# Performance work log

Measured on AMD Instinct MI355X. Metric: run time of the kernel, lower is better.

The kernel has to match this reference:

```python
import jax, jax.numpy as jnp
import numpy as np

N_NODES = 10000
N_EDGES = 640000
IN_FEATS = 128
OUT_FEATS = 128


def setup_inputs() -> dict:
    key = jax.random.key(0)
    k1, k2, k3, k4, k5 = jax.random.split(key, 5)
    x = jax.random.normal(k1, (N_NODES, IN_FEATS), dtype=jnp.float32)
    src = jax.random.randint(k2, (N_EDGES,), 0, N_NODES, dtype=jnp.int64)
    dst = jax.random.randint(k3, (N_EDGES,), 0, N_NODES, dtype=jnp.int64)
    # nn.Linear(in_feats, out_feats): weight [out, in], bias [out]
    bound = 1.0 / np.sqrt(IN_FEATS)
    W = jax.random.uniform(k4, (OUT_FEATS, IN_FEATS), minval=-bound, maxval=bound, dtype=jnp.float32)
    b = jax.random.uniform(k5, (OUT_FEATS,), minval=-bound, maxval=bound, dtype=jnp.float32)
    return {"x": x, "src": src, "dst": dst, "W": W, "b": b}


def reference(x, src, dst, W, b):
    # DGL GINConv (eps=0, sum aggregator): rst = (1+eps)*x + sum_{j->i} x_j, then Linear
    agg = jax.ops.segment_sum(x[src], dst, num_segments=N_NODES)  # [N, in]
    h = x + agg
    return h @ W.T + b  # [N, out]
```

## Files before the change

### kernel.cpp

```cpp
#include <hip/hip_runtime.h>

#define N_NODES 10000
#define N_EDGES 640000
#define FEATS 128
#define NBKT 625
#define CAPB 2048
#define GSTRIDE 16
#define GEMM_WAVES 625
#define GEMM_GRID 157
#define P1_BLOCKS 79
#define WCVT_BLOCKS 16
#define XCVT_BLOCKS 1250
#define CLR_BLOCKS 40

typedef __attribute__((ext_vector_type(8))) short short8;
typedef __attribute__((ext_vector_type(4))) float f32x4;

static __device__ __forceinline__ unsigned short f2bf(float f) {
    unsigned int u = __float_as_uint(f);
    u = (u + 0x7FFFu + ((u >> 16) & 1u)) >> 16;
    return (unsigned short)u;
}
static __device__ __forceinline__ float bf2f(unsigned short h) {
    return __uint_as_float((unsigned int)h << 16);
}

__global__ void prep_kernel(const float* __restrict__ x,
                            const float* __restrict__ W,
                            unsigned short* __restrict__ xhi,
                            unsigned short* __restrict__ xlo,
                            unsigned short* __restrict__ wb,
                            int* __restrict__ gcur) {
    int blk = blockIdx.x;
    int tid = threadIdx.x;
    if (blk < WCVT_BLOCKS) {
        int i = blk * 256 + tid;
        float4 v = reinterpret_cast<const float4*>(W)[i];
        ushort4 h;
        h.x = f2bf(v.x); h.y = f2bf(v.y); h.z = f2bf(v.z); h.w = f2bf(v.w);
        reinterpret_cast<ushort4*>(wb)[i] = h;
    } else if (blk < WCVT_BLOCKS + XCVT_BLOCKS) {
        int i = (blk - WCVT_BLOCKS) * 256 + tid;
        float4 v = reinterpret_cast<const float4*>(x)[i];
        ushort4 h, l;
        h.x = f2bf(v.x); h.y = f2bf(v.y); h.z = f2bf(v.z); h.w = f2bf(v.w);
        l.x = f2bf(v.x - bf2f(h.x)); l.y = f2bf(v.y - bf2f(h.y));
        l.z = f2bf(v.z - bf2f(h.z)); l.w = f2bf(v.w - bf2f(h.w));
        reinterpret_cast<ushort4*>(xhi)[i] = h;
        reinterpret_cast<ushort4*>(xlo)[i] = l;
    } else {
        int i = (blk - WCVT_BLOCKS - XCVT_BLOCKS) * 256 + tid;
        if (i < NBKT * GSTRIDE) gcur[i] = 0;
    }
}

__global__ __launch_bounds__(256) void fused_kernel(const unsigned short* __restrict__ xhi,
                                                    const unsigned short* __restrict__ xlo,
                                                    const unsigned short* __restrict__ wb,
                                                    const int* __restrict__ src,
                                                    const int* __restrict__ dst,
                                                    unsigned short* __restrict__ ybf,
                                                    int* __restrict__ gcur,
                                                    int* __restrict__ ebuf) {
    __shared__ int lhist[NBKT];
    __shared__ int sbase[NBKT];
    __shared__ int lcur[NBKT];
    int tid = threadIdx.x;

    if (blockIdx.x < GEMM_GRID) {
        int wave = blockIdx.x * 4 + (tid >> 6);
        if (wave >= GEMM_WAVES) return;
        int lane = tid & 63;
        int m0 = wave * 16;
        int mrow = m0 + (lane & 15);
        int kbase = (lane >> 4) * 8;

        short8 ahi[4], alo[4];
        #pragma unroll
        for (int c = 0; c < 4; ++c) {
            ahi[c] = *reinterpret_cast<const short8*>(xhi + mrow * FEATS + c * 32 + kbase);
            alo[c] = *reinterpret_cast<const short8*>(xlo + mrow * FEATS + c * 32 + kbase);
        }

        int nr = lane & 15;
        int rbase = m0 + (lane >> 4) * 4;
        #pragma unroll
        for (int t = 0; t < 8; ++t) {
            f32x4 acc = {0.f, 0.f, 0.f, 0.f};
            #pragma unroll
            for (int c = 0; c < 4; ++c) {
                short8 bf = *reinterpret_cast<const short8*>(wb + (t * 16 + nr) * FEATS + c * 32 + kbase);
                acc = __builtin_amdgcn_mfma_f32_16x16x32_bf16(ahi[c], bf, acc, 0, 0, 0);
                acc = __builtin_amdgcn_mfma_f32_16x16x32_bf16(alo[c], bf, acc, 0, 0, 0);
            }
            int col = t * 16 + (lane & 15);
            #pragma unroll
            for (int r = 0; r < 4; ++r) {
                ybf[(rbase + r) * FEATS + col] = f2bf(acc[r]);
            }
        }
        return;
    }

    int blk = blockIdx.x - GEMM_GRID;
    for (int i = tid; i < NBKT; i += 256) lhist[i] = 0;
    __syncthreads();

    const int4* dst4 = reinterpret_cast<const int4*>(dst);
    const int4* src4 = reinterpret_cast<const int4*>(src);
    int i4base = blk * 2048;

    #pragma unroll
    for (int j = 0; j < 8; ++j) {
        int i4 = i4base + j * 256 + tid;
        if (i4 < N_EDGES / 4) {
            int4 d = dst4[i4];
            atomicAdd(&lhist[d.x >> 4], 1);
            atomicAdd(&lhist[d.y >> 4], 1);
            atomicAdd(&lhist[d.z >> 4], 1);
            atomicAdd(&lhist[d.w >> 4], 1);
        }
    }
    __syncthreads();

    for (int i = tid; i < NBKT; i += 256) {
        int c = lhist[i];
        int base = c ? atomicAdd(&gcur[i * GSTRIDE], c) : 0;
        sbase[i] = i * CAPB + base;
        lcur[i] = 0;
    }
    __syncthreads();

    #pragma unroll
    for (int j = 0; j < 8; ++j) {
        int i4 = i4base + j * 256 + tid;
        if (i4 < N_EDGES / 4) {
            int4 d = dst4[i4];
            int4 s = src4[i4];
            int b0 = d.x >> 4, b1 = d.y >> 4, b2 = d.z >> 4, b3 = d.w >> 4;
            int p0 = atomicAdd(&lcur[b0], 1);
            int p1 = atomicAdd(&lcur[b1], 1);
            int p2 = atomicAdd(&lcur[b2], 1);
            int p3 = atomicAdd(&lcur[b3], 1);
            int a0 = sbase[b0] + p0; if (a0 < (b0 + 1) * CAPB) ebuf[a0] = ((d.x & 15) << 16) | s.x;
            int a1 = sbase[b1] + p1; if (a1 < (b1 + 1) * CAPB) ebuf[a1] = ((d.y & 15) << 16) | s.y;
            int a2 = sbase[b2] + p2; if (a2 < (b2 + 1) * CAPB) ebuf[a2] = ((d.z & 15) << 16) | s.z;
            int a3 = sbase[b3] + p3; if (a3 < (b3 + 1) * CAPB) ebuf[a3] = ((d.w & 15) << 16) | s.w;
        }
    }
}

__global__ __launch_bounds__(1024) void pass2_kernel(const unsigned short* __restrict__ ybf,
                                                     const int* __restrict__ ebuf,
                                                     const int* __restrict__ gcur,
                                                     const float* __restrict__ b,
                                                     float* __restrict__ out) {
    __shared__ int q2[CAPB];
    __shared__ int cnts[16];
    __shared__ int offs[17];
    __shared__ int curs[16];
    int bkt = blockIdx.x;
    int tid = threadIdx.x;

    int cnt = gcur[bkt * GSTRIDE];
    if (cnt > CAPB) cnt = CAPB;
    if (cnt < 0) cnt = 0;
    if (tid < 16) cnts[tid] = 0;
    __syncthreads();

    const int* eb = ebuf + bkt * CAPB;
    for (int i = tid; i < cnt; i += 1024) atomicAdd(&cnts[(eb[i] >> 16) & 15], 1);
    __syncthreads();

    if (tid == 0) {
        int a = 0;
        #pragma unroll
        for (int l = 0; l < 16; ++l) { offs[l] = a; curs[l] = a; a += cnts[l]; }
        offs[16] = a;
    }
    __syncthreads();

    for (int i = tid; i < cnt; i += 1024) {
        int v = eb[i];
        int p = atomicAdd(&curs[(v >> 16) & 15], 1);
        q2[p] = v & 0xFFFF;
    }
    __syncthreads();

    int w = tid >> 6;
    int lane = tid & 63;
    int s0 = offs[w];
    int s1 = offs[w + 1];

    float ax = 0.f, ay = 0.f;
    int i = s0;
    for (; i + 8 <= s1; i += 8) {
        int sA[8];
        #pragma unroll
        for (int j = 0; j < 8; ++j) sA[j] = q2[i + j];
        #pragma unroll
        for (int j = 0; j < 8; ++j) {
            ushort2 v = *reinterpret_cast<const ushort2*>(ybf + sA[j] * FEATS + lane * 2);
            ax += bf2f(v.x); ay += bf2f(v.y);
        }
    }
    for (; i < s1; ++i) {
        int s = q2[i];
        ushort2 v = *reinterpret_cast<const ushort2*>(ybf + s * FEATS + lane * 2);
        ax += bf2f(v.x); ay += bf2f(v.y);
    }

    int node = bkt * 16 + w;
    ushort2 sv = *reinterpret_cast<const ushort2*>(ybf + node * FEATS + lane * 2);
    float2 bs = reinterpret_cast<const float2*>(b)[lane];
    float2 o;
    o.x = ax + bf2f(sv.x) + bs.x;
    o.y = ay + bf2f(sv.y) + bs.y;
    reinterpret_cast<float2*>(out + node * FEATS)[lane] = o;
}

extern "C" void kernel_launch(void* const* d_in, const int* in_sizes, int n_in,
                              void* d_out, int out_size, void* d_ws, size_t ws_size,
                              hipStream_t stream) {
    const float* x   = (const float*)d_in[0];
    const int*   src = (const int*)d_in[1];
    const int*   dst = (const int*)d_in[2];
    const float* W   = (const float*)d_in[3];
    const float* b   = (const float*)d_in[4];
    float* out = (float*)d_out;

    unsigned short* xhi = (unsigned short*)d_ws;
    unsigned short* xlo = xhi + N_NODES * FEATS;
    unsigned short* wb  = xlo + N_NODES * FEATS;
    unsigned short* ybf = wb + FEATS * FEATS;
    int* gcur = (int*)(ybf + N_NODES * FEATS);
    int* ebuf = gcur + NBKT * GSTRIDE;

    prep_kernel<<<WCVT_BLOCKS + XCVT_BLOCKS + CLR_BLOCKS, 256, 0, stream>>>(x, W, xhi, xlo, wb, gcur);
    fused_kernel<<<GEMM_GRID + P1_BLOCKS, 256, 0, stream>>>(xhi, xlo, wb, src, dst, ybf, gcur, ebuf);
    pass2_kernel<<<NBKT, 1024, 0, stream>>>(ybf, ebuf, gcur, b, out);
}
```

Baseline: 98.60 us.

## Fuse x hi/lo bf16 split into GEMM waves and split output columns across waves

Removes the separate x-to-bf16 hi/lo conversion pass from the prep kernel. The GEMM waves now read fp32 x directly and split it into registers. The GEMM is also re-tiled so that each wave computes half the output columns (64) with four independent accumulators, and the wave count is doubled. This drops the xhi/xlo round trip through global memory and raises MFMA-level parallelism. In exchange, each x row is read and converted twice, once per column half.

```diff
diff --git a/kernel.cpp b/kernel.cpp
--- a/kernel.cpp
+++ b/kernel.cpp
@@ -6,11 +6,10 @@
 #define NBKT 625
 #define CAPB 2048
 #define GSTRIDE 16
-#define GEMM_WAVES 625
-#define GEMM_GRID 157
+#define GEMM_WAVES 1250
+#define GEMM_GRID 313
 #define P1_BLOCKS 79
 #define WCVT_BLOCKS 16
-#define XCVT_BLOCKS 1250
 #define CLR_BLOCKS 40
 
 typedef __attribute__((ext_vector_type(8))) short short8;
@@ -25,10 +24,7 @@
     return __uint_as_float((unsigned int)h << 16);
 }
 
-__global__ void prep_kernel(const float* __restrict__ x,
-                            const float* __restrict__ W,
-                            unsigned short* __restrict__ xhi,
-                            unsigned short* __restrict__ xlo,
+__global__ void prep_kernel(const float* __restrict__ W,
                             unsigned short* __restrict__ wb,
                             int* __restrict__ gcur) {
     int blk = blockIdx.x;
@@ -39,23 +35,13 @@
         ushort4 h;
         h.x = f2bf(v.x); h.y = f2bf(v.y); h.z = f2bf(v.z); h.w = f2bf(v.w);
         reinterpret_cast<ushort4*>(wb)[i] = h;
-    } else if (blk < WCVT_BLOCKS + XCVT_BLOCKS) {
+    } else {
         int i = (blk - WCVT_BLOCKS) * 256 + tid;
-        float4 v = reinterpret_cast<const float4*>(x)[i];
-        ushort4 h, l;
-        h.x = f2bf(v.x); h.y = f2bf(v.y); h.z = f2bf(v.z); h.w = f2bf(v.w);
-        l.x = f2bf(v.x - bf2f(h.x)); l.y = f2bf(v.y - bf2f(h.y));
-        l.z = f2bf(v.z - bf2f(h.z)); l.w = f2bf(v.w - bf2f(h.w));
-        reinterpret_cast<ushort4*>(xhi)[i] = h;
-        reinterpret_cast<ushort4*>(xlo)[i] = l;
-    } else {
-        int i = (blk - WCVT_BLOCKS - XCVT_BLOCKS) * 256 + tid;
         if (i < NBKT * GSTRIDE) gcur[i] = 0;
     }
 }
 
-__global__ __launch_bounds__(256) void fused_kernel(const unsigned short* __restrict__ xhi,
-                                                    const unsigned short* __restrict__ xlo,
+__global__ __launch_bounds__(256) void fused_kernel(const float* __restrict__ x,
                                                     const unsigned short* __restrict__ wb,
                                                     const int* __restrict__ src,
                                                     const int* __restrict__ dst,
@@ -71,32 +57,53 @@
         int wave = blockIdx.x * 4 + (tid >> 6);
         if (wave >= GEMM_WAVES) return;
         int lane = tid & 63;
-        int m0 = wave * 16;
+        int mtile = wave >> 1;
+        int chalf = (wave & 1) * 64;
+        int m0 = mtile * 16;
         int mrow = m0 + (lane & 15);
         int kbase = (lane >> 4) * 8;
 
         short8 ahi[4], alo[4];
         #pragma unroll
         for (int c = 0; c < 4; ++c) {
-            ahi[c] = *reinterpret_cast<const short8*>(xhi + mrow * FEATS + c * 32 + kbase);
-            alo[c] = *reinterpret_cast<const short8*>(xlo + mrow * FEATS + c * 32 + kbase);
+            const float* xp = x + mrow * FEATS + c * 32 + kbase;
+            float4 v0 = *reinterpret_cast<const float4*>(xp);
+            float4 v1 = *reinterpret_cast<const float4*>(xp + 4);
+            float f[8] = {v0.x, v0.y, v0.z, v0.w, v1.x, v1.y, v1.z, v1.w};
+            #pragma unroll
+            for (int j = 0; j < 8; ++j) {
+                unsigned short h = f2bf(f[j]);
+                ahi[c][j] = (short)h;
+                alo[c][j] = (short)f2bf(f[j] - bf2f(h));
+            }
         }
 
         int nr = lane & 15;
         int rbase = m0 + (lane >> 4) * 4;
-        #pragma unroll
-        for (int t = 0; t < 8; ++t) {
-            f32x4 acc = {0.f, 0.f, 0.f, 0.f};
-            #pragma unroll
-            for (int c = 0; c < 4; ++c) {
-                short8 bf = *reinterpret_cast<const short8*>(wb + (t * 16 + nr) * FEATS + c * 32 + kbase);
-                acc = __builtin_amdgcn_mfma_f32_16x16x32_bf16(ahi[c], bf, acc, 0, 0, 0);
-                acc = __builtin_amdgcn_mfma_f32_16x16x32_bf16(alo[c], bf, acc, 0, 0, 0);
+        f32x4 accs[4] = {{0.f,0.f,0.f,0.f},{0.f,0.f,0.f,0.f},
+                         {0.f,0.f,0.f,0.f},{0.f,0.f,0.f,0.f}};
+        #pragma unroll
+        for (int c = 0; c < 4; ++c) {
+            short8 bfr[4];
+            #pragma unroll
+            for (int t = 0; t < 4; ++t) {
+                int n = chalf + t * 16 + nr;
+                bfr[t] = *reinterpret_cast<const short8*>(wb + n * FEATS + c * 32 + kbase);
             }
-            int col = t * 16 + (lane & 15);
+            #pragma unroll
+            for (int t = 0; t < 4; ++t)
+                accs[t] = __builtin_amdgcn_mfma_f32_16x16x32_bf16(ahi[c], bfr[t], accs[t], 0, 0, 0);
+            #pragma unroll
+            for (int t = 0; t < 4; ++t)
+                accs[t] = __builtin_amdgcn_mfma_f32_16x16x32_bf16(alo[c], bfr[t], accs[t], 0, 0, 0);
+        }
+
+        #pragma unroll
+        for (int t = 0; t < 4; ++t) {
+            int col = chalf + t * 16 + (lane & 15);
             #pragma unroll
             for (int r = 0; r < 4; ++r) {
-                ybf[(rbase + r) * FEATS + col] = f2bf(acc[r]);
+                ybf[(rbase + r) * FEATS + col] = f2bf(accs[t][r]);
             }
         }
         return;
@@ -229,14 +236,12 @@
     const float* b   = (const float*)d_in[4];
     float* out = (float*)d_out;
 
-    unsigned short* xhi = (unsigned short*)d_ws;
-    unsigned short* xlo = xhi + N_NODES * FEATS;
-    unsigned short* wb  = xlo + N_NODES * FEATS;
+    unsigned short* wb  = (unsigned short*)d_ws;
     unsigned short* ybf = wb + FEATS * FEATS;
     int* gcur = (int*)(ybf + N_NODES * FEATS);
     int* ebuf = gcur + NBKT * GSTRIDE;
 
-    prep_kernel<<<WCVT_BLOCKS + XCVT_BLOCKS + CLR_BLOCKS, 256, 0, stream>>>(x, W, xhi, xlo, wb, gcur);
-    fused_kernel<<<GEMM_GRID + P1_BLOCKS, 256, 0, stream>>>(xhi, xlo, wb, src, dst, ybf, gcur, ebuf);
+    prep_kernel<<<WCVT_BLOCKS + CLR_BLOCKS, 256, 0, stream>>>(W, wb, gcur);
+    fused_kernel<<<GEMM_GRID + P1_BLOCKS, 256, 0, stream>>>(x, wb, src, dst, ybf, gcur, ebuf);
     pass2_kernel<<<NBKT, 1024, 0, stream>>>(ybf, ebuf, gcur, b, out);
 }
```

Measured after the change: 99.18 us. No clear change (+0.6%).
